# Kernel tuning notes

Measured on AMD Instinct MI355X. Metric: run time of the kernel, lower is better.

## Reference

```python
import jax, jax.numpy as jnp
import numpy as np

NUM_FREQS = 12  # fourfeat_config
EMB_DIM = 3 + 6 * NUM_FREQS  # identity + sin/cos per freq per dim = 75


def fourier_ipe(x, cov, decay):
    # x: [N,3], cov: [N,3,3], decay: scalar (coarse-to-fine window cutoff)
    N = x.shape[0]
    freqs = 2.0 ** jnp.arange(NUM_FREQS, dtype=jnp.float32)            # [F]
    xb = x[:, None, :] * freqs[:, None]                                # [N,F,3]
    var = jnp.diagonal(cov, axis1=-2, axis2=-1)[:, None, :] * (freqs ** 2)[:, None]  # [N,F,3]
    # nerfies-style cosine easing window per frequency band
    window = 0.5 * (1.0 - jnp.cos(jnp.pi * jnp.clip(decay - jnp.arange(NUM_FREQS, dtype=jnp.float32), 0.0, 1.0)))  # [F]
    atten = jnp.exp(-0.5 * var) * window[:, None]                      # [N,F,3]
    four = jnp.concatenate([jnp.sin(xb), jnp.cos(xb)], axis=-1) * jnp.concatenate([atten, atten], axis=-1)  # [N,F,6]
    return jnp.concatenate([x, four.reshape(N, 6 * NUM_FREQS)], axis=-1)  # [N,75]


def mlp(h, W_in, b_in, W_hid, b_hid, W_out, b_out):
    h = jax.nn.relu(h @ W_in + b_in)
    for i in range(W_hid.shape[0]):  # fixed small layer count
        h = jax.nn.relu(h @ W_hid[i] + b_hid[i])
    return h @ W_out + b_out  # output_activation = None


def setup_inputs() -> dict:
    key = jax.random.key(0)
    ks = jax.random.split(key, 16)
    bshape = (2, 16384, 8)
    mean = jax.random.normal(ks[0], (*bshape, 3), jnp.float32)
    cov = jax.random.uniform(ks[1], (*bshape, 3, 3), jnp.float32) * 1e-4  # small positive diag

    def w(k, shp):
        return jax.random.normal(k, shp, jnp.float32) / np.sqrt(shp[-2]).astype(np.float32)

    FD, FC = 256, 128  # features_density, features_color
    HD, HC = 8 - 2, 4 - 2  # n_hidden_layers = layers - 2
    return {
        'mean': mean, 'cov': cov,
        'Wd_in': w(ks[2], (EMB_DIM, FD)), 'bd_in': jnp.zeros((FD,), jnp.float32),
        'Wd_hid': w(ks[3], (HD, FD, FD)), 'bd_hid': jnp.zeros((HD, FD), jnp.float32),
        'Wd_out': w(ks[4], (FD, FD + 1)), 'bd_out': jnp.zeros((FD + 1,), jnp.float32),
        'Wc_in': w(ks[5], (FD, FC)), 'bc_in': jnp.zeros((FC,), jnp.float32),
        'Wc_hid': w(ks[6], (HC, FC, FC)), 'bc_hid': jnp.zeros((HC, FC), jnp.float32),
        'Wc_out': w(ks[7], (FC, 3)), 'bc_out': jnp.zeros((3,), jnp.float32),
        'decayscale': 12,
    }


def reference(mean, cov, Wd_in, bd_in, Wd_hid, bd_hid, Wd_out, bd_out,
              Wc_in, bc_in, Wc_hid, bc_hid, Wc_out, bc_out, decayscale):
    batch_shape = mean.shape[:-1]
    N = int(np.prod(batch_shape))
    x = mean.reshape(N, 3)
    c = cov.reshape(N, 3, 3)
    emb = fourier_ipe(x, c, jnp.float32(decayscale))                    # [N,75]
    feat = mlp(emb, Wd_in, bd_in, Wd_hid, bd_hid, Wd_out, bd_out)       # [N,257]
    d, features = feat[:, :1], feat[:, 1:]
    # parameterization == 'VolSDF' (capitalized) -> no SDF radius offset branch
    raw_rgb = mlp(features, Wc_in, bc_in, Wc_hid, bc_hid, Wc_out, bc_out)  # [N,3]
    raw = jnp.concatenate([raw_rgb, d], axis=-1)                        # [N,4]
    return raw.reshape(*batch_shape, 4)
```

## Files before the change

kernel.cpp:

```cpp
#include <hip/hip_runtime.h>
#include <hip/hip_bf16.h>

#define PI_F 3.14159265358979323846f
#define KPAD 260

typedef _Float16 h8 __attribute__((ext_vector_type(8)));
typedef _Float16 h4 __attribute__((ext_vector_type(4)));
typedef _Float16 h2 __attribute__((ext_vector_type(2)));
typedef __fp16 fp16x2 __attribute__((ext_vector_type(2)));
typedef float f32x16 __attribute__((ext_vector_type(16)));

__device__ __forceinline__ h2 cvt_pk_h2(float a, float b)
{
    fp16x2 r = __builtin_amdgcn_cvt_pkrtz(a, b);
    return __builtin_bit_cast(h2, r);
}

#define OFF_DIN   0
#define OFF_DHID  24576
#define OFF_FEAT  417792
#define OFF_CIN   483328
#define OFF_CHID  516096
#define OFF_COUT  548864
#define W_TOTAL   552960
#define FB_DIN  0
#define FB_DHID 256
#define FB_FEAT 1792
#define FB_CIN  2048
#define FB_CHID 2176
#define FB_WD0  2432
#define FB_BD0  2688
#define B_TOTAL 2689
#define PREP_TOTAL (W_TOTAL + B_TOTAL)

__global__ void prep_kernel(const float* __restrict__ Wd_in,  const float* __restrict__ Wd_hid,
                            const float* __restrict__ Wd_out, const float* __restrict__ Wc_in,
                            const float* __restrict__ Wc_hid, const float* __restrict__ Wc_out,
                            const float* __restrict__ bd_in,  const float* __restrict__ bd_hid,
                            const float* __restrict__ bd_out, const float* __restrict__ bc_in,
                            const float* __restrict__ bc_hid,
                            _Float16* __restrict__ wdst, float* __restrict__ bdst)
{
    int i = blockIdx.x * 256 + threadIdx.x;
    if (i >= PREP_TOTAL) return;
    if (i < W_TOTAL) {
        float v = 0.f;
        int j, n, k;
        #define DECODE(jj, KTv)  do { int frag = (jj) >> 3; int e = (jj) & 7;          \
                                      int lane = frag & 63; int tk = frag >> 6;         \
                                      int ntl = tk / (KTv); int kt = tk % (KTv);        \
                                      n = ntl * 32 + (lane & 31);                       \
                                      k = kt * 16 + (lane >> 5) * 8 + e; } while (0)
        if (i < OFF_DHID) {
            j = i; DECODE(j, 6);
            if (k < 75) v = Wd_in[k * 256 + n];
        } else if (i < OFF_FEAT) {
            j = i - OFF_DHID; int l = j >> 16; j &= 65535; DECODE(j, 16);
            v = Wd_hid[(l * 256 + k) * 256 + n];
        } else if (i < OFF_CIN) {
            j = i - OFF_FEAT; DECODE(j, 16);
            v = Wd_out[k * 257 + n + 1];
        } else if (i < OFF_CHID) {
            j = i - OFF_CIN; DECODE(j, 16);
            v = Wc_in[k * 128 + n];
        } else if (i < OFF_COUT) {
            j = i - OFF_CHID; int l = j >> 14; j &= 16383; DECODE(j, 8);
            v = Wc_hid[(l * 128 + k) * 128 + n];
        } else {
            j = i - OFF_COUT; DECODE(j, 8);
            if (n < 3) v = Wc_out[k * 3 + n];
        }
        #undef DECODE
        wdst[i] = (_Float16)v;
    } else {
        int b = i - W_TOTAL;
        float v = 0.f;
        #define BDECODE(bb) int ntl = (bb) >> 5; int r5 = (bb) & 31;                   \
                            int lq = r5 >> 4, jj = r5 & 15;                            \
                            int n = ntl * 32 + (jj & 3) + 8 * (jj >> 2) + 4 * lq
        if (b < FB_DHID)      { BDECODE(b); v = bd_in[n]; }
        else if (b < FB_FEAT) { int b2 = b - FB_DHID; int l = b2 >> 8; int bb = b2 & 255;
                                BDECODE(bb); v = bd_hid[l * 256 + n]; }
        else if (b < FB_CIN)  { int bb = b - FB_FEAT; BDECODE(bb); v = bd_out[n + 1]; }
        else if (b < FB_CHID) { int bb = b - FB_CIN; BDECODE(bb); v = bc_in[n]; }
        else if (b < FB_WD0)  { int b2 = b - FB_CHID; int l = b2 >> 7; int bb = b2 & 127;
                                BDECODE(bb); v = bc_hid[l * 128 + n]; }
        else if (b < FB_BD0)  { int k = b - FB_WD0; v = Wd_out[k * 257]; }
        else                  { v = bd_out[0]; }
        #undef BDECODE
        bdst[b] = v;
    }
}

__device__ __forceinline__ h8 lds_read_h8(const _Float16* p)
{
    h4 lo = *(const h4*)(p);
    h4 hi = *(const h4*)(p + 4);
    return __builtin_shufflevector(lo, hi, 0, 1, 2, 3, 4, 5, 6, 7);
}

template<int KT, int NT, bool RELU, bool DDOT>
__device__ __forceinline__ void dense(_Float16 (*At)[KPAD],
                                      const _Float16* __restrict__ WP,
                                      const float* __restrict__ bfrag,
                                      const float* __restrict__ wd0,
                                      float (*dpart)[64],
                                      int c, int lrow, int lq, int lane)
{
    const int ntile0 = c * NT;
    f32x16 acc[2][NT];
#pragma unroll
    for (int nt = 0; nt < NT; ++nt) {
        f32x16 b = *(const f32x16*)(bfrag + (ntile0 + nt) * 32 + lq * 16);
        acc[0][nt] = b;
        acc[1][nt] = b;
    }

    const _Float16* wbase = WP + ((size_t)ntile0 * KT) * 512 + (size_t)lane * 8;

#pragma unroll 2
    for (int kt = 0; kt < KT; ++kt) {
        const int koff = kt * 16 + lq * 8;
        h8 wf[NT];
#pragma unroll
        for (int nt = 0; nt < NT; ++nt)
            wf[nt] = *(const h8*)(wbase + (size_t)(nt * KT + kt) * 512);
        h8 af[2];
#pragma unroll
        for (int mt = 0; mt < 2; ++mt)
            af[mt] = lds_read_h8(&At[mt * 32 + lrow][koff]);
        __builtin_amdgcn_s_setprio(1);
#pragma unroll
        for (int mt = 0; mt < 2; ++mt)
#pragma unroll
            for (int nt = 0; nt < NT; ++nt)
                acc[mt][nt] = __builtin_amdgcn_mfma_f32_32x32x16_f16(wf[nt], af[mt], acc[mt][nt], 0, 0, 0);
        __builtin_amdgcn_s_setprio(0);
    }

    if (DDOT) {
        float s = 0.f;
        const float* w0 = wd0 + c * 64;
#pragma unroll
        for (int kk = 0; kk < 64; kk += 8) {
            h8 hv = lds_read_h8(&At[lane][c * 64 + kk]);
#pragma unroll
            for (int e = 0; e < 8; ++e)
                s = fmaf((float)hv[e], w0[kk + e], s);
        }
        dpart[c][lane] = s;
    }

    __syncthreads();

#pragma unroll
    for (int mt = 0; mt < 2; ++mt) {
        const int m = mt * 32 + lrow;
#pragma unroll
        for (int nt = 0; nt < NT; ++nt) {
#pragma unroll
            for (int p = 0; p < 4; ++p) {
                const int n0 = (ntile0 + nt) * 32 + p * 8 + lq * 4;
                h2 lo = cvt_pk_h2(acc[mt][nt][4 * p + 0], acc[mt][nt][4 * p + 1]);
                h2 hi = cvt_pk_h2(acc[mt][nt][4 * p + 2], acc[mt][nt][4 * p + 3]);
                h4 hv = __builtin_shufflevector(lo, hi, 0, 1, 2, 3);
                if (RELU) {
                    const h4 zero = {(_Float16)0, (_Float16)0, (_Float16)0, (_Float16)0};
                    hv = __builtin_elementwise_max(hv, zero);
                }
                *(h4*)(&At[m][n0]) = hv;
            }
        }
    }
    __syncthreads();
}

__global__ __launch_bounds__(256, 4)
void ffmlp_kernel(const float* __restrict__ mean, const float* __restrict__ cov,
                  const int* __restrict__ decayscale,
                  const _Float16* __restrict__ wws, const float* __restrict__ bws,
                  const float* __restrict__ bc_out,
                  float* __restrict__ out, int N)
{
    __shared__ __align__(16) _Float16 At[64][KPAD];
    __shared__ float dpart[4][64];

    const int t = threadIdx.x;
    const int c = t >> 6, lane = t & 63;
    const int lrow = lane & 31, lq = lane >> 5;
    const int p0 = blockIdx.x * 64;

    {
        const int m = t >> 2, q = t & 3;
        const long pt = (long)p0 + m;
        float x0 = 0.f, x1 = 0.f, x2 = 0.f, v0 = 0.f, v1 = 0.f, v2 = 0.f;
        if (pt < N) {
            x0 = mean[pt * 3 + 0]; x1 = mean[pt * 3 + 1]; x2 = mean[pt * 3 + 2];
            v0 = cov[pt * 9 + 0];  v1 = cov[pt * 9 + 4];  v2 = cov[pt * 9 + 8];
        }
        const float dec = (float)(*decayscale);
        if (q == 0) {
            At[m][0] = (_Float16)x0; At[m][1] = (_Float16)x1; At[m][2] = (_Float16)x2;
            for (int k = 75; k < 80; ++k) At[m][k] = (_Float16)0.f;
        } else {
            for (int k = 75 + 5 * q; k < (q == 3 ? 96 : 80 + 5 * q); ++k) At[m][k] = (_Float16)0.f;
        }
        const float xs[3] = {x0, x1, x2}, vs[3] = {v0, v1, v2};
#pragma unroll
        for (int fi = 0; fi < 3; ++fi) {
            const int f = q * 3 + fi;
            const float fs = (float)(1 << f);
            const float wcl = fminf(fmaxf(dec - (float)f, 0.f), 1.f);
            const float win = 0.5f * (1.f - cosf(wcl * PI_F));
#pragma unroll
            for (int d = 0; d < 3; ++d) {
                const float xb = xs[d] * fs;
                const float att = expf(-0.5f * vs[d] * fs * fs) * win;
                float s, co;
                sincosf(xb, &s, &co);
                At[m][3 + 6 * f + d] = (_Float16)(s * att);
                At[m][6 + 6 * f + d] = (_Float16)(co * att);
            }
        }
    }
    __syncthreads();

    dense<6, 2, true, false>(At, wws + OFF_DIN, bws + FB_DIN, bws, dpart, c, lrow, lq, lane);
#pragma unroll 1
    for (int i = 0; i < 6; ++i)
        dense<16, 2, true, false>(At, wws + OFF_DHID + i * 65536, bws + FB_DHID + i * 256,
                                  bws, dpart, c, lrow, lq, lane);
    dense<16, 2, false, true>(At, wws + OFF_FEAT, bws + FB_FEAT, bws + FB_WD0, dpart, c, lrow, lq, lane);

    dense<16, 1, true, false>(At, wws + OFF_CIN, bws + FB_CIN, bws, dpart, c, lrow, lq, lane);
#pragma unroll 1
    for (int i = 0; i < 2; ++i)
        dense<8, 1, true, false>(At, wws + OFF_CHID + i * 16384, bws + FB_CHID + i * 128,
                                 bws, dpart, c, lrow, lq, lane);

    if (c == 0) {
        f32x16 acc[2];
#pragma unroll
        for (int mt = 0; mt < 2; ++mt)
#pragma unroll
            for (int j = 0; j < 16; ++j) acc[mt][j] = 0.f;
        const _Float16* wco = wws + OFF_COUT + (size_t)lane * 8;
#pragma unroll
        for (int kt = 0; kt < 8; ++kt) {
            const int koff = kt * 16 + lq * 8;
            h8 wf = *(const h8*)(wco + (size_t)kt * 512);
#pragma unroll
            for (int mt = 0; mt < 2; ++mt) {
                h8 af = lds_read_h8(&At[mt * 32 + lrow][koff]);
                acc[mt] = __builtin_amdgcn_mfma_f32_32x32x16_f16(wf, af, acc[mt], 0, 0, 0);
            }
        }
        const float bc0 = bc_out[0], bc1 = bc_out[1], bc2 = bc_out[2];
        const float bd0 = bws[FB_BD0];
        if (lq == 0) {
#pragma unroll
            for (int mt = 0; mt < 2; ++mt) {
                const int m = mt * 32 + lrow;
                const long pt = (long)p0 + m;
                if (pt < N) {
                    float4 o;
                    o.x = acc[mt][0] + bc0;
                    o.y = acc[mt][1] + bc1;
                    o.z = acc[mt][2] + bc2;
                    o.w = dpart[0][m] + dpart[1][m] + dpart[2][m] + dpart[3][m] + bd0;
                    *(float4*)(out + pt * 4) = o;
                }
            }
        }
    }
}

extern "C" void kernel_launch(void* const* d_in, const int* in_sizes, int n_in,
                              void* d_out, int out_size, void* d_ws, size_t ws_size,
                              hipStream_t stream)
{
    const float* mean   = (const float*)d_in[0];
    const float* cov    = (const float*)d_in[1];
    const float* Wd_in  = (const float*)d_in[2];
    const float* bd_in  = (const float*)d_in[3];
    const float* Wd_hid = (const float*)d_in[4];
    const float* bd_hid = (const float*)d_in[5];
    const float* Wd_out = (const float*)d_in[6];
    const float* bd_out = (const float*)d_in[7];
    const float* Wc_in  = (const float*)d_in[8];
    const float* bc_in  = (const float*)d_in[9];
    const float* Wc_hid = (const float*)d_in[10];
    const float* bc_hid = (const float*)d_in[11];
    const float* Wc_out = (const float*)d_in[12];
    const float* bc_out = (const float*)d_in[13];
    const int*   decay  = (const int*)d_in[14];

    _Float16* wws = (_Float16*)d_ws;
    float*    bws = (float*)((char*)d_ws + (size_t)W_TOTAL * 2);

    const int N = in_sizes[0] / 3;

    const int prep_blocks = (PREP_TOTAL + 255) / 256;
    prep_kernel<<<prep_blocks, 256, 0, stream>>>(Wd_in, Wd_hid, Wd_out, Wc_in, Wc_hid, Wc_out,
                                                 bd_in, bd_hid, bd_out, bc_in, bc_hid, wws, bws);

    const int blocks = (N + 63) / 64;
    ffmlp_kernel<<<blocks, 256, 0, stream>>>(mean, cov, decay, wws, bws, bc_out, (float*)d_out, N);
}
```

Before: 315.1 us.

## Double-buffer activation LDS and prefetch next layer weights across layers

Activations now ping-pong between two LDS buffers, so each layer writes its output to the other buffer. This removes one of the two block barriers per layer, and the remaining barrier only waits on LDS counters. The first two k-steps of the next layer's weights are loaded into registers before the current layer's epilogue, hiding global load latency at layer boundaries. The k-loop is fully unrolled and launch bounds drop to 2 blocks per SM. The costs are doubled LDS per block and more register pressure, which may reduce occupancy.

```diff
diff --git a/kernel.cpp b/kernel.cpp
--- a/kernel.cpp
+++ b/kernel.cpp
@@ -14,6 +14,13 @@
 {
     fp16x2 r = __builtin_amdgcn_cvt_pkrtz(a, b);
     return __builtin_bit_cast(h2, r);
+}
+
+__device__ __forceinline__ void lgkm_barrier()
+{
+    asm volatile("s_waitcnt lgkmcnt(0)" ::: "memory");
+    __builtin_amdgcn_sched_barrier(0);
+    __builtin_amdgcn_s_barrier();
 }
 
 #define OFF_DIN   0
@@ -99,13 +106,30 @@
     return __builtin_shufflevector(lo, hi, 0, 1, 2, 3, 4, 5, 6, 7);
 }
 
-template<int KT, int NT, bool RELU, bool DDOT>
-__device__ __forceinline__ void dense(_Float16 (*At)[KPAD],
+template<int NT>
+__device__ __forceinline__ void kt_step(_Float16 (*Ac)[KPAD], int koff, int lrow,
+                                        const h8* wf, f32x16 (*acc)[NT])
+{
+    h8 af0 = lds_read_h8(&Ac[lrow][koff]);
+    h8 af1 = lds_read_h8(&Ac[32 + lrow][koff]);
+    __builtin_amdgcn_s_setprio(1);
+    acc[0][0] = __builtin_amdgcn_mfma_f32_32x32x16_f16(wf[0], af0, acc[0][0], 0, 0, 0);
+    acc[1][0] = __builtin_amdgcn_mfma_f32_32x32x16_f16(wf[0], af1, acc[1][0], 0, 0, 0);
+    if constexpr (NT == 2) {
+        acc[0][1] = __builtin_amdgcn_mfma_f32_32x32x16_f16(wf[1], af0, acc[0][1], 0, 0, 0);
+        acc[1][1] = __builtin_amdgcn_mfma_f32_32x32x16_f16(wf[1], af1, acc[1][1], 0, 0, 0);
+    }
+    __builtin_amdgcn_s_setprio(0);
+}
+
+template<int KT, int NT, bool RELU, bool DDOT, bool PFIN, bool PFOUT, int KTN, int NTN>
+__device__ __forceinline__ void dense(_Float16 (*Ac)[KPAD], _Float16 (*An)[KPAD],
                                       const _Float16* __restrict__ WP,
                                       const float* __restrict__ bfrag,
                                       const float* __restrict__ wd0,
                                       float (*dpart)[64],
-                                      int c, int lrow, int lq, int lane)
+                                      int c, int lrow, int lq, int lane,
+                                      h8* pf, const _Float16* __restrict__ WPn)
 {
     const int ntile0 = c * NT;
     f32x16 acc[2][NT];
@@ -118,24 +142,38 @@
 
     const _Float16* wbase = WP + ((size_t)ntile0 * KT) * 512 + (size_t)lane * 8;
 
-#pragma unroll 2
-    for (int kt = 0; kt < KT; ++kt) {
-        const int koff = kt * 16 + lq * 8;
+    {
+        h8 w0[NT], w1[NT];
+        if constexpr (PFIN) {
+            w0[0] = pf[0]; w1[0] = pf[1];
+            if constexpr (NT == 2) { w0[1] = pf[2]; w1[1] = pf[3]; }
+        } else {
+#pragma unroll
+            for (int nt = 0; nt < NT; ++nt) {
+                w0[nt] = *(const h8*)(wbase + (size_t)(nt * KT + 0) * 512);
+                w1[nt] = *(const h8*)(wbase + (size_t)(nt * KT + 1) * 512);
+            }
+        }
+        kt_step<NT>(Ac, 0 * 16 + lq * 8, lrow, w0, acc);
+        kt_step<NT>(Ac, 1 * 16 + lq * 8, lrow, w1, acc);
+    }
+#pragma unroll
+    for (int kt = 2; kt < KT; ++kt) {
         h8 wf[NT];
 #pragma unroll
         for (int nt = 0; nt < NT; ++nt)
             wf[nt] = *(const h8*)(wbase + (size_t)(nt * KT + kt) * 512);
-        h8 af[2];
-#pragma unroll
-        for (int mt = 0; mt < 2; ++mt)
-            af[mt] = lds_read_h8(&At[mt * 32 + lrow][koff]);
-        __builtin_amdgcn_s_setprio(1);
-#pragma unroll
-        for (int mt = 0; mt < 2; ++mt)
-#pragma unroll
-            for (int nt = 0; nt < NT; ++nt)
-                acc[mt][nt] = __builtin_amdgcn_mfma_f32_32x32x16_f16(wf[nt], af[mt], acc[mt][nt], 0, 0, 0);
-        __builtin_amdgcn_s_setprio(0);
+        kt_step<NT>(Ac, kt * 16 + lq * 8, lrow, wf, acc);
+    }
+
+    if constexpr (PFOUT) {
+        const _Float16* wn = WPn + ((size_t)(c * NTN) * KTN) * 512 + (size_t)lane * 8;
+        pf[0] = *(const h8*)(wn);
+        pf[1] = *(const h8*)(wn + 512);
+        if constexpr (NTN == 2) {
+            pf[2] = *(const h8*)(wn + (size_t)KTN * 512);
+            pf[3] = *(const h8*)(wn + (size_t)(KTN + 1) * 512);
+        }
     }
 
     if (DDOT) {
@@ -143,15 +181,13 @@
         const float* w0 = wd0 + c * 64;
 #pragma unroll
         for (int kk = 0; kk < 64; kk += 8) {
-            h8 hv = lds_read_h8(&At[lane][c * 64 + kk]);
+            h8 hv = lds_read_h8(&Ac[lane][c * 64 + kk]);
 #pragma unroll
             for (int e = 0; e < 8; ++e)
                 s = fmaf((float)hv[e], w0[kk + e], s);
         }
         dpart[c][lane] = s;
     }
-
-    __syncthreads();
 
 #pragma unroll
     for (int mt = 0; mt < 2; ++mt) {
@@ -168,22 +204,24 @@
                     const h4 zero = {(_Float16)0, (_Float16)0, (_Float16)0, (_Float16)0};
                     hv = __builtin_elementwise_max(hv, zero);
                 }
-                *(h4*)(&At[m][n0]) = hv;
-            }
-        }
-    }
-    __syncthreads();
-}
-
-__global__ __launch_bounds__(256, 4)
+                *(h4*)(&An[m][n0]) = hv;
+            }
+        }
+    }
+    lgkm_barrier();
+}
+
+__global__ __launch_bounds__(256, 2)
 void ffmlp_kernel(const float* __restrict__ mean, const float* __restrict__ cov,
                   const int* __restrict__ decayscale,
                   const _Float16* __restrict__ wws, const float* __restrict__ bws,
                   const float* __restrict__ bc_out,
                   float* __restrict__ out, int N)
 {
-    __shared__ __align__(16) _Float16 At[64][KPAD];
-    __shared__ float dpart[4][64];
+    extern __shared__ __align__(16) char smem[];
+    _Float16 (*At0)[KPAD] = (_Float16 (*)[KPAD])smem;
+    _Float16 (*At1)[KPAD] = (_Float16 (*)[KPAD])(smem + 64 * KPAD * 2);
+    float (*dpart)[64]    = (float (*)[64])(smem + 2 * 64 * KPAD * 2);
 
     const int t = threadIdx.x;
     const int c = t >> 6, lane = t & 63;
@@ -200,10 +238,10 @@
         }
         const float dec = (float)(*decayscale);
         if (q == 0) {
-            At[m][0] = (_Float16)x0; At[m][1] = (_Float16)x1; At[m][2] = (_Float16)x2;
-            for (int k = 75; k < 80; ++k) At[m][k] = (_Float16)0.f;
+            At0[m][0] = (_Float16)x0; At0[m][1] = (_Float16)x1; At0[m][2] = (_Float16)x2;
+            for (int k = 75; k < 80; ++k) At0[m][k] = (_Float16)0.f;
         } else {
-            for (int k = 75 + 5 * q; k < (q == 3 ? 96 : 80 + 5 * q); ++k) At[m][k] = (_Float16)0.f;
+            for (int k = 75 + 5 * q; k < (q == 3 ? 96 : 80 + 5 * q); ++k) At0[m][k] = (_Float16)0.f;
         }
         const float xs[3] = {x0, x1, x2}, vs[3] = {v0, v1, v2};
 #pragma unroll
@@ -218,25 +256,43 @@
                 const float att = expf(-0.5f * vs[d] * fs * fs) * win;
                 float s, co;
                 sincosf(xb, &s, &co);
-                At[m][3 + 6 * f + d] = (_Float16)(s * att);
-                At[m][6 + 6 * f + d] = (_Float16)(co * att);
+                At0[m][3 + 6 * f + d] = (_Float16)(s * att);
+                At0[m][6 + 6 * f + d] = (_Float16)(co * att);
             }
         }
     }
     __syncthreads();
 
-    dense<6, 2, true, false>(At, wws + OFF_DIN, bws + FB_DIN, bws, dpart, c, lrow, lq, lane);
+    h8 pf[4];
+    _Float16 (*Ac)[KPAD] = At0, (*An)[KPAD] = At1;
+
+    dense<6, 2, true, false, false, true, 16, 2>(Ac, An, wws + OFF_DIN, bws + FB_DIN, bws,
+                                                 dpart, c, lrow, lq, lane, pf, wws + OFF_DHID);
+    { auto tmp = Ac; Ac = An; An = tmp; }
 #pragma unroll 1
-    for (int i = 0; i < 6; ++i)
-        dense<16, 2, true, false>(At, wws + OFF_DHID + i * 65536, bws + FB_DHID + i * 256,
-                                  bws, dpart, c, lrow, lq, lane);
-    dense<16, 2, false, true>(At, wws + OFF_FEAT, bws + FB_FEAT, bws + FB_WD0, dpart, c, lrow, lq, lane);
-
-    dense<16, 1, true, false>(At, wws + OFF_CIN, bws + FB_CIN, bws, dpart, c, lrow, lq, lane);
-#pragma unroll 1
-    for (int i = 0; i < 2; ++i)
-        dense<8, 1, true, false>(At, wws + OFF_CHID + i * 16384, bws + FB_CHID + i * 128,
-                                 bws, dpart, c, lrow, lq, lane);
+    for (int i = 0; i < 6; ++i) {
+        const _Float16* wpn = (i < 5) ? (wws + OFF_DHID + (i + 1) * 65536) : (wws + OFF_FEAT);
+        dense<16, 2, true, false, true, true, 16, 2>(Ac, An, wws + OFF_DHID + i * 65536,
+                                                     bws + FB_DHID + i * 256, bws,
+                                                     dpart, c, lrow, lq, lane, pf, wpn);
+        { auto tmp = Ac; Ac = An; An = tmp; }
+    }
+    dense<16, 2, false, true, true, true, 16, 1>(Ac, An, wws + OFF_FEAT, bws + FB_FEAT,
+                                                 bws + FB_WD0, dpart, c, lrow, lq, lane,
+                                                 pf, wws + OFF_CIN);
+    { auto tmp = Ac; Ac = An; An = tmp; }
+
+    dense<16, 1, true, false, true, true, 8, 1>(Ac, An, wws + OFF_CIN, bws + FB_CIN, bws,
+                                                dpart, c, lrow, lq, lane, pf, wws + OFF_CHID);
+    { auto tmp = Ac; Ac = An; An = tmp; }
+    dense<8, 1, true, false, true, true, 8, 1>(Ac, An, wws + OFF_CHID, bws + FB_CHID, bws,
+                                               dpart, c, lrow, lq, lane, pf,
+                                               wws + OFF_CHID + 16384);
+    { auto tmp = Ac; Ac = An; An = tmp; }
+    dense<8, 1, true, false, true, false, 8, 1>(Ac, An, wws + OFF_CHID + 16384,
+                                                bws + FB_CHID + 128, bws,
+                                                dpart, c, lrow, lq, lane, pf, nullptr);
+    { auto tmp = Ac; Ac = An; An = tmp; }
 
     if (c == 0) {
         f32x16 acc[2];
@@ -251,7 +307,7 @@
             h8 wf = *(const h8*)(wco + (size_t)kt * 512);
 #pragma unroll
             for (int mt = 0; mt < 2; ++mt) {
-                h8 af = lds_read_h8(&At[mt * 32 + lrow][koff]);
+                h8 af = lds_read_h8(&Ac[mt * 32 + lrow][koff]);
                 acc[mt] = __builtin_amdgcn_mfma_f32_32x32x16_f16(wf, af, acc[mt], 0, 0, 0);
             }
         }
@@ -274,6 +330,8 @@
         }
     }
 }
+
+#define LDS_BYTES (2 * 64 * KPAD * 2 + 4 * 64 * 4)
 
 extern "C" void kernel_launch(void* const* d_in, const int* in_sizes, int n_in,
                               void* d_out, int out_size, void* d_ws, size_t ws_size,
@@ -300,10 +358,14 @@
 
     const int N = in_sizes[0] / 3;
 
+    (void)hipFuncSetAttribute((const void*)ffmlp_kernel,
+                              hipFuncAttributeMaxDynamicSharedMemorySize, LDS_BYTES);
+
     const int prep_blocks = (PREP_TOTAL + 255) / 256;
     prep_kernel<<<prep_blocks, 256, 0, stream>>>(Wd_in, Wd_hid, Wd_out, Wc_in, Wc_hid, Wc_out,
                                                  bd_in, bd_hid, bd_out, bc_in, bc_hid, wws, bws);
 
     const int blocks = (N + 63) / 64;
-    ffmlp_kernel<<<blocks, 256, 0, stream>>>(mean, cov, decay, wws, bws, bc_out, (float*)d_out, N);
-}
+    ffmlp_kernel<<<blocks, 256, LDS_BYTES, stream>>>(mean, cov, decay, wws, bws, bc_out,
+                                                     (float*)d_out, N);
+}
```

New measurement: 338.8 us. 1.07x slower.

## Prefetch weight fragments three k-steps ahead via buffer loads with explicit vmcnt waits

Applied to the files above, without the earlier changes.

Replaces the plain global weight loads in the dense layer loop with raw buffer_load_dwordx4 instructions into a 4-deep register ring. Each load is issued three k-tiles ahead, and an explicit s_waitcnt vmcnt lets the MFMAs for the current tile run while later weights are still in flight. The k loop is fully unrolled through template recursion. Launch bounds drop from 4 to 3 blocks per SM to leave registers for the prefetch buffers, at the cost of lower occupancy and hand-managed wait counts that could break if the compiler inserts other memory ops.

```diff
diff --git a/kernel.cpp b/kernel.cpp
--- a/kernel.cpp
+++ b/kernel.cpp
@@ -9,11 +9,42 @@
 typedef _Float16 h2 __attribute__((ext_vector_type(2)));
 typedef __fp16 fp16x2 __attribute__((ext_vector_type(2)));
 typedef float f32x16 __attribute__((ext_vector_type(16)));
+typedef unsigned int u32x4 __attribute__((ext_vector_type(4)));
 
 __device__ __forceinline__ h2 cvt_pk_h2(float a, float b)
 {
     fp16x2 r = __builtin_amdgcn_cvt_pkrtz(a, b);
     return __builtin_bit_cast(h2, r);
+}
+
+__device__ __forceinline__ u32x4 make_srsrc(const void* p, unsigned bytes)
+{
+    unsigned long long a = (unsigned long long)p;
+    u32x4 r;
+    r.x = (unsigned)a;
+    r.y = (unsigned)(a >> 32);
+    r.z = bytes;
+    r.w = 0x00020000u;
+    return r;
+}
+
+template<int N>
+__device__ __forceinline__ void vm_wait()
+{
+    if constexpr (N >= 6)      asm volatile("s_waitcnt vmcnt(6)" ::: "memory");
+    else if constexpr (N == 5) asm volatile("s_waitcnt vmcnt(5)" ::: "memory");
+    else if constexpr (N == 4) asm volatile("s_waitcnt vmcnt(4)" ::: "memory");
+    else if constexpr (N == 3) asm volatile("s_waitcnt vmcnt(3)" ::: "memory");
+    else if constexpr (N == 2) asm volatile("s_waitcnt vmcnt(2)" ::: "memory");
+    else if constexpr (N == 1) asm volatile("s_waitcnt vmcnt(1)" ::: "memory");
+    else                       asm volatile("s_waitcnt vmcnt(0)" ::: "memory");
+    __builtin_amdgcn_sched_barrier(0);
+}
+
+__device__ __forceinline__ void issue_wf(float4& d, unsigned voff, u32x4 rs)
+{
+    asm volatile("buffer_load_dwordx4 %0, %1, %2, 0 offen"
+                 : "=v"(d) : "v"(voff), "s"(rs) : "memory");
 }
 
 #define OFF_DIN   0
@@ -99,9 +130,38 @@
     return __builtin_shufflevector(lo, hi, 0, 1, 2, 3, 4, 5, 6, 7);
 }
 
+template<int KT, int NT, int KTI>
+__device__ __forceinline__ void kt_iter(_Float16 (*At)[KPAD], u32x4 rs,
+                                        unsigned bo, int lrow, int lq,
+                                        float4 (*wq)[NT], f32x16 (*acc)[NT])
+{
+    if constexpr (KTI >= KT) {
+        return;
+    } else {
+        constexpr int D = 3;
+        if constexpr (KTI + D < KT) {
+#pragma unroll
+            for (int nt = 0; nt < NT; ++nt)
+                issue_wf(wq[(KTI + D) & 3][nt],
+                         bo + (unsigned)((nt * KT + KTI + D) * 1024), rs);
+        }
+        const int koff = KTI * 16 + lq * 8;
+        h8 af0 = lds_read_h8(&At[lrow][koff]);
+        h8 af1 = lds_read_h8(&At[32 + lrow][koff]);
+        constexpr int AHEAD = ((KT - 1 - KTI) < D) ? (KT - 1 - KTI) : D;
+        vm_wait<NT * AHEAD>();
+#pragma unroll
+        for (int nt = 0; nt < NT; ++nt) {
+            h8 w = __builtin_bit_cast(h8, wq[KTI & 3][nt]);
+            acc[0][nt] = __builtin_amdgcn_mfma_f32_32x32x16_f16(w, af0, acc[0][nt], 0, 0, 0);
+            acc[1][nt] = __builtin_amdgcn_mfma_f32_32x32x16_f16(w, af1, acc[1][nt], 0, 0, 0);
+        }
+        kt_iter<KT, NT, KTI + 1>(At, rs, bo, lrow, lq, wq, acc);
+    }
+}
+
 template<int KT, int NT, bool RELU, bool DDOT>
-__device__ __forceinline__ void dense(_Float16 (*At)[KPAD],
-                                      const _Float16* __restrict__ WP,
+__device__ __forceinline__ void dense(_Float16 (*At)[KPAD], u32x4 rs, unsigned wboff,
                                       const float* __restrict__ bfrag,
                                       const float* __restrict__ wd0,
                                       float (*dpart)[64],
@@ -116,27 +176,16 @@
         acc[1][nt] = b;
     }
 
-    const _Float16* wbase = WP + ((size_t)ntile0 * KT) * 512 + (size_t)lane * 8;
-
-#pragma unroll 2
-    for (int kt = 0; kt < KT; ++kt) {
-        const int koff = kt * 16 + lq * 8;
-        h8 wf[NT];
+    const unsigned bo = wboff + (unsigned)(ntile0 * KT) * 1024u + (unsigned)(lane * 16);
+    float4 wq[4][NT];
+
+#pragma unroll
+    for (int kt = 0; kt < 3; ++kt)
 #pragma unroll
         for (int nt = 0; nt < NT; ++nt)
-            wf[nt] = *(const h8*)(wbase + (size_t)(nt * KT + kt) * 512);
-        h8 af[2];
-#pragma unroll
-        for (int mt = 0; mt < 2; ++mt)
-            af[mt] = lds_read_h8(&At[mt * 32 + lrow][koff]);
-        __builtin_amdgcn_s_setprio(1);
-#pragma unroll
-        for (int mt = 0; mt < 2; ++mt)
-#pragma unroll
-            for (int nt = 0; nt < NT; ++nt)
-                acc[mt][nt] = __builtin_amdgcn_mfma_f32_32x32x16_f16(wf[nt], af[mt], acc[mt][nt], 0, 0, 0);
-        __builtin_amdgcn_s_setprio(0);
-    }
+            issue_wf(wq[kt][nt], bo + (unsigned)((nt * KT + kt) * 1024), rs);
+
+    kt_iter<KT, NT, 0>(At, rs, bo, lrow, lq, wq, acc);
 
     if (DDOT) {
         float s = 0.f;
@@ -175,7 +224,7 @@
     __syncthreads();
 }
 
-__global__ __launch_bounds__(256, 4)
+__global__ __launch_bounds__(256, 3)
 void ffmlp_kernel(const float* __restrict__ mean, const float* __restrict__ cov,
                   const int* __restrict__ decayscale,
                   const _Float16* __restrict__ wws, const float* __restrict__ bws,
@@ -189,6 +238,7 @@
     const int c = t >> 6, lane = t & 63;
     const int lrow = lane & 31, lq = lane >> 5;
     const int p0 = blockIdx.x * 64;
+    const u32x4 rs = make_srsrc(wws, (unsigned)W_TOTAL * 2u);
 
     {
         const int m = t >> 2, q = t & 3;
@@ -225,17 +275,18 @@
     }
     __syncthreads();
 
-    dense<6, 2, true, false>(At, wws + OFF_DIN, bws + FB_DIN, bws, dpart, c, lrow, lq, lane);
+    dense<6, 2, true, false>(At, rs, OFF_DIN * 2u, bws + FB_DIN, bws, dpart, c, lrow, lq, lane);
 #pragma unroll 1
     for (int i = 0; i < 6; ++i)
-        dense<16, 2, true, false>(At, wws + OFF_DHID + i * 65536, bws + FB_DHID + i * 256,
+        dense<16, 2, true, false>(At, rs, (OFF_DHID + i * 65536) * 2u, bws + FB_DHID + i * 256,
                                   bws, dpart, c, lrow, lq, lane);
-    dense<16, 2, false, true>(At, wws + OFF_FEAT, bws + FB_FEAT, bws + FB_WD0, dpart, c, lrow, lq, lane);
-
-    dense<16, 1, true, false>(At, wws + OFF_CIN, bws + FB_CIN, bws, dpart, c, lrow, lq, lane);
+    dense<16, 2, false, true>(At, rs, OFF_FEAT * 2u, bws + FB_FEAT, bws + FB_WD0, dpart,
+                              c, lrow, lq, lane);
+
+    dense<16, 1, true, false>(At, rs, OFF_CIN * 2u, bws + FB_CIN, bws, dpart, c, lrow, lq, lane);
 #pragma unroll 1
     for (int i = 0; i < 2; ++i)
-        dense<8, 1, true, false>(At, wws + OFF_CHID + i * 16384, bws + FB_CHID + i * 128,
+        dense<8, 1, true, false>(At, rs, (OFF_CHID + i * 16384) * 2u, bws + FB_CHID + i * 128,
                                  bws, dpart, c, lrow, lq, lane);
 
     if (c == 0) {
```

After: 286.3 us. 1.1x faster.
